# Kernel optimization log

Measured on AMD Instinct MI355X. Metric: run time of the kernel, lower is better.

The kernel has to match this reference:

```python
import jax, jax.numpy as jnp
import numpy as np

V, H, L, B, S = 32000, 1024, 2, 32, 512

def setup_inputs() -> dict:
    key = jax.random.key(0)
    ks = jax.random.split(key, 24)
    g = lambda k, shp, s=0.02: jax.random.normal(k, shp, dtype=jnp.float32) * s
    inp = {
        'input_ids': jax.random.randint(ks[0], (1, B), 0, V),
        'hidden': jax.random.normal(ks[1], (L, B, H), dtype=jnp.float32),
        'encoder_output': jax.random.normal(ks[2], (S, B, H), dtype=jnp.float32),
        'encoder_output_pinyin': jax.random.normal(ks[3], (S, B, H), dtype=jnp.float32),
        'embedding': g(ks[4], (V, H), 1.0),
        'W_ih0': g(ks[5], (3 * H, H)), 'W_hh0': g(ks[6], (3 * H, H)),
        'b_ih0': jnp.zeros((3 * H,), jnp.float32), 'b_hh0': jnp.zeros((3 * H,), jnp.float32),
        'W_ih1': g(ks[7], (3 * H, H)), 'W_hh1': g(ks[8], (3 * H, H)),
        'b_ih1': jnp.zeros((3 * H,), jnp.float32), 'b_hh1': jnp.zeros((3 * H,), jnp.float32),
        'att_fc1_w': g(ks[9], (H, 3 * H)), 'att_fc1_b': jnp.zeros((H,), jnp.float32),
        'att_fc2_w': g(ks[10], (1, H)), 'att_fc2_b': jnp.zeros((1,), jnp.float32),
        'attp_fc1_w': g(ks[11], (H, 3 * H)), 'attp_fc1_b': jnp.zeros((H,), jnp.float32),
        'attp_fc2_w': g(ks[12], (1, H)), 'attp_fc2_b': jnp.zeros((1,), jnp.float32),
        'attn_fc_w': g(ks[13], (H, 3 * H)), 'attn_fc_b': jnp.zeros((H,), jnp.float32),
        'fc_w': g(ks[14], (V, H)), 'fc_b': jnp.zeros((V,), jnp.float32),
    }
    return inp


def _gru_cell(x, h, Wih, Whh, bih, bhh):
    # torch GRU gate order: r, z, n
    gi = x @ Wih.T + bih          # [B, 3H]
    gh = h @ Whh.T + bhh          # [B, 3H]
    ir, iz, in_ = jnp.split(gi, 3, axis=-1)
    hr, hz, hn = jnp.split(gh, 3, axis=-1)
    r = jax.nn.sigmoid(ir + hr)
    z = jax.nn.sigmoid(iz + hz)
    n = jnp.tanh(in_ + r * hn)
    return (1.0 - z) * n + z * h


def _attention(hidden, enc, fc1_w, fc1_b, fc2_w, fc2_b):
    # hidden: [L, B, H], enc: [S, B, H]
    s, b = enc.shape[0], enc.shape[1]
    state = jnp.transpose(hidden, (1, 0, 2)).reshape(b, -1)       # [B, L*H]
    enc_b = jnp.transpose(enc, (1, 0, 2))                          # [B, S, H]
    state_rep = jnp.broadcast_to(state[:, None, :], (b, s, state.shape[-1]))
    concat = jnp.concatenate([state_rep, enc_b], axis=-1)          # [B, S, 3H]
    energy = jnp.tanh(concat @ fc1_w.T + fc1_b)                    # [B, S, H]
    energy = (energy @ fc2_w.T + fc2_b).transpose(0, 2, 1)         # [B, 1, S]
    alpha = jax.nn.softmax(energy, axis=2)
    context = jnp.einsum('bis,bsh->bih', alpha, enc_b)             # [B, 1, H]
    return jnp.transpose(context, (1, 0, 2)), alpha                # [1, B, H]


def reference(input_ids, hidden, encoder_output, encoder_output_pinyin, embedding,
              W_ih0, W_hh0, b_ih0, b_hh0, W_ih1, W_hh1, b_ih1, b_hh1,
              att_fc1_w, att_fc1_b, att_fc2_w, att_fc2_b,
              attp_fc1_w, attp_fc1_b, attp_fc2_w, attp_fc2_b,
              attn_fc_w, attn_fc_b, fc_w, fc_b):
    embedded = embedding[input_ids]             # [1, B, H] (dropout: eval mode = identity)
    x = embedded[0]                             # [B, H]
    h0 = _gru_cell(x, hidden[0], W_ih0, W_hh0, b_ih0, b_hh0)
    h1 = _gru_cell(h0, hidden[1], W_ih1, W_hh1, b_ih1, b_hh1)
    new_hidden = jnp.stack([h0, h1], axis=0)    # [L, B, H]
    output = h1[None]                           # [1, B, H]
    context, _ = _attention(new_hidden, encoder_output, att_fc1_w, att_fc1_b, att_fc2_w, att_fc2_b)
    context_p, _ = _attention(new_hidden, encoder_output_pinyin, attp_fc1_w, attp_fc1_b, attp_fc2_w, attp_fc2_b)
    fused = jnp.concatenate([output, context, context_p], axis=2)  # [1, B, 3H]
    output = jax.nn.relu(fused @ attn_fc_w.T + attn_fc_b)          # [1, B, H]
    logits = output @ fc_w.T + fc_b                                # [1, B, V]
    return logits, new_hidden
```

## Files before the change

### kernel.cpp

```cpp
#include <hip/hip_runtime.h>
#include <math.h>

#define Bsz 32
#define Hd  1024
#define Sd  512
#define Vd  32000

typedef __attribute__((ext_vector_type(8))) short v8s;
typedef __attribute__((ext_vector_type(4))) float v4f;

__device__ __forceinline__ float sigf(float x){ return 1.0f/(1.0f+__expf(-x)); }
__device__ __forceinline__ float ftanh(float x){
  float e = __expf(2.0f*x);
  return 1.0f - 2.0f/(e+1.0f);
}
__device__ __forceinline__ unsigned pk(float lo, float hi){
  return __builtin_amdgcn_perm(__float_as_uint(hi), __float_as_uint(lo), 0x07060302u);
}

__global__ void k_cvt_fc1w(const float* __restrict__ aw, const float* __restrict__ pw,
                           ushort* __restrict__ ab, ushort* __restrict__ pb){
  int tt = blockIdx.x*256 + threadIdx.x;
  int idx = tt*8;
  int s = idx >> 20;
  int r = idx & 1048575;
  int j = r >> 10, k = r & 1023;
  const float* src = (s? pw : aw) + (size_t)j*3072 + 2048 + k;
  float4 f0 = *(const float4*)src, f1 = *(const float4*)(src+4);
  uint4 p = { pk(f0.x,f0.y), pk(f0.z,f0.w), pk(f1.x,f1.y), pk(f1.z,f1.w) };
  *(uint4*)((s? pb : ab) + r) = p;
}

__global__ void k_embed(const int* __restrict__ ids, const float* __restrict__ emb,
                        float* __restrict__ x){
  int t = blockIdx.x*256 + threadIdx.x;
  int b = t >> 10, k = t & (Hd-1);
  x[t] = emb[(size_t)ids[b]*Hd + k];
}

__global__ void k_gates9(const float* __restrict__ x, const float* __restrict__ hid,
                         const float* __restrict__ Wih0, const float* __restrict__ Whh0,
                         const float* __restrict__ Whh1, float* __restrict__ gA){
  int blk = blockIdx.x;
  int g  = blk >> 9;
  int kc = (blk >> 7) & 3;
  int tt = (blk & 127)*256 + threadIdx.x;
  int b = tt & 31, j = tt >> 5;
  const float* vec; const float* w;
  if (g < 3){ vec = x + b*Hd; w = Wih0 + ((size_t)(g*Hd + j))*Hd; }
  else if (g < 6){ vec = hid + b*Hd; w = Whh0 + ((size_t)((g-3)*Hd + j))*Hd; }
  else { vec = hid + Bsz*Hd + b*Hd; w = Whh1 + ((size_t)((g-6)*Hd + j))*Hd; }
  const float4* v4 = (const float4*)(vec + kc*256);
  const float4* w4 = (const float4*)(w + kc*256);
  float acc = 0.f;
  #pragma unroll 8
  for (int k=0;k<64;k++){ float4 a=v4[k], ww=w4[k];
    acc += a.x*ww.x+a.y*ww.y+a.z*ww.z+a.w*ww.w; }
  atomicAdd(&gA[(size_t)g*32768 + j*32 + b], acc);
}

__global__ void k_gates3(const float* __restrict__ h0, const float* __restrict__ Wih1,
                         float* __restrict__ gB){
  int blk = blockIdx.x;
  int g  = blk >> 9;
  int kc = (blk >> 7) & 3;
  int tt = (blk & 127)*256 + threadIdx.x;
  int b = tt & 31, j = tt >> 5;
  const float4* v4 = (const float4*)(h0 + b*Hd + kc*256);
  const float4* w4 = (const float4*)(Wih1 + ((size_t)(g*Hd + j))*Hd + kc*256);
  float acc = 0.f;
  #pragma unroll 8
  for (int k=0;k<64;k++){ float4 a=v4[k], ww=w4[k];
    acc += a.x*ww.x+a.y*ww.y+a.z*ww.z+a.w*ww.w; }
  atomicAdd(&gB[(size_t)g*32768 + j*32 + b], acc);
}

__global__ void k_gru_comb(const float* __restrict__ xg, const float* __restrict__ hg,
                           const float* __restrict__ h, const float* __restrict__ bih,
                           const float* __restrict__ bhh, float* __restrict__ hnew){
  int tt = blockIdx.x*256 + threadIdx.x;
  int b = tt & 31, j = tt >> 5;
  float ir = xg[tt], iz = xg[32768 + tt], in_ = xg[2*32768 + tt];
  float hr = hg[tt], hz = hg[32768 + tt], hn  = hg[2*32768 + tt];
  float r = sigf(ir + bih[j]      + hr + bhh[j]);
  float z = sigf(iz + bih[Hd+j]   + hz + bhh[Hd+j]);
  float n = ftanh(in_ + bih[2*Hd+j] + r*(hn + bhh[2*Hd+j]));
  hnew[(size_t)b*Hd + j] = (1.f-z)*n + z*h[(size_t)b*Hd + j];
}

__global__ void k_spsplit(const float* __restrict__ h0, const float* __restrict__ h1,
                          const float* __restrict__ afc1w, const float* __restrict__ pfc1w,
                          float* __restrict__ spa_, float* __restrict__ spp_){
  int blk = blockIdx.x;
  int s  = blk >> 9;
  int kc = (blk >> 7) & 3;
  int tt = (blk & 127)*256 + threadIdx.x;
  int b = tt & 31, j = tt >> 5;
  const float* w = (s? pfc1w : afc1w) + (size_t)j*3*Hd + kc*512;
  const float* vec = (kc < 2 ? h0 : h1) + b*Hd + (kc & 1)*512;
  const float4* v4 = (const float4*)vec;
  const float4* w4 = (const float4*)w;
  float acc = 0.f;
  #pragma unroll 8
  for (int k=0;k<128;k++){ float4 a=v4[k], ww=w4[k];
    acc += a.x*ww.x+a.y*ww.y+a.z*ww.z+a.w*ww.w; }
  atomicAdd((s? spp_ : spa_) + (size_t)b*Hd + j, acc);
}

__global__ __launch_bounds__(256, 2)
void k_att_mfma(const float* __restrict__ enc0, const float* __restrict__ enc1,
                const ushort* __restrict__ wb0, const ushort* __restrict__ wb1,
                const float* __restrict__ sp0, const float* __restrict__ sp1,
                const float* __restrict__ b10, const float* __restrict__ b11,
                const float* __restrict__ w20, const float* __restrict__ w21,
                float* __restrict__ e0, float* __restrict__ e1){
  const int z = blockIdx.z;
  const float*  enc = z? enc1 : enc0;
  const ushort* wb  = z? wb1  : wb0;
  const float*  sp  = z? sp1  : sp0;
  const float*  b1  = z? b11  : b10;
  const float*  fc2 = z? w21  : w20;
  float* e = z? e1 : e0;
  __shared__ __align__(16) ushort As[128*72];
  __shared__ __align__(16) ushort Bs[128*72];
  const int t = threadIdx.x;
  const int lane = t & 63;
  const int w = t >> 6;
  const int wm = w >> 1, wn = w & 1;
  const int q = lane >> 4, c15 = lane & 15;
  const int row0 = blockIdx.y * 128;
  const int col0 = blockIdx.x * 128;

  const int lrow = t >> 3, lkp = (t & 7)*8;
  const float* gA = enc + (size_t)(row0 + lrow)*Hd + lkp;
  const int brow = t >> 1, bkp = (t & 1)*32;
  const ushort* gB = wb + (size_t)(col0 + brow)*Hd + bkp;

  v4f acc[4][4];
  for (int mi=0;mi<4;mi++) for (int ni=0;ni<4;ni++) acc[mi][ni] = (v4f){0.f,0.f,0.f,0.f};

  for (int k0 = 0; k0 < Hd; k0 += 64){
    #pragma unroll
    for (int i = 0; i < 4; i++){
      const float* p = gA + (size_t)i*32*Hd + k0;
      float4 a0 = *(const float4*)p;
      float4 a1 = *(const float4*)(p+4);
      uint4 pa = { pk(a0.x,a0.y), pk(a0.z,a0.w), pk(a1.x,a1.y), pk(a1.z,a1.w) };
      *(uint4*)&As[(i*32 + lrow)*72 + lkp] = pa;
    }
    {
      const uint4* pb4 = (const uint4*)(gB + k0);
      uint4 b0_=pb4[0], b1_=pb4[1], b2_=pb4[2], b3_=pb4[3];
      uint4* d = (uint4*)&Bs[brow*72 + bkp];
      d[0]=b0_; d[1]=b1_; d[2]=b2_; d[3]=b3_;
    }
    __syncthreads();
    #pragma unroll
    for (int kk = 0; kk < 2; kk++){
      v8s af[4], bf[4];
      #pragma unroll
      for (int mi=0;mi<4;mi++)
        af[mi] = *(const v8s*)&As[(wm*64 + mi*16 + c15)*72 + kk*32 + q*8];
      #pragma unroll
      for (int ni=0;ni<4;ni++)
        bf[ni] = *(const v8s*)&Bs[(wn*64 + ni*16 + c15)*72 + kk*32 + q*8];
      #pragma unroll
      for (int mi=0;mi<4;mi++)
        #pragma unroll
        for (int ni=0;ni<4;ni++)
          acc[mi][ni] = __builtin_amdgcn_mfma_f32_16x16x32_bf16(af[mi], bf[ni], acc[mi][ni], 0, 0, 0);
    }
    __syncthreads();
  }

  #pragma unroll
  for (int mi=0;mi<4;mi++){
    float rs[4] = {0.f,0.f,0.f,0.f};
    #pragma unroll
    for (int ni=0;ni<4;ni++){
      int col = col0 + wn*64 + ni*16 + c15;
      float w2 = fc2[col];
      float bb1 = b1[col];
      int bb = (mi & 1) * 16;
      #pragma unroll
      for (int r=0;r<4;r++){
        int b = bb + q*4 + r;
        float xv = acc[mi][ni][r] + sp[(size_t)b*Hd + col] + bb1;
        rs[r] += w2 * ftanh(xv);
      }
    }
    #pragma unroll
    for (int r=0;r<4;r++){
      float v = rs[r];
      v += __shfl_xor(v, 1);
      v += __shfl_xor(v, 2);
      v += __shfl_xor(v, 4);
      v += __shfl_xor(v, 8);
      if (c15 == 0)
        atomicAdd(&e[row0 + wm*64 + mi*16 + q*4 + r], v);
    }
  }
}

__global__ void k_softmax(float* __restrict__ ea_, float* __restrict__ ep_){
  float* e = blockIdx.y ? ep_ : ea_;
  const int b = blockIdx.x, t = threadIdx.x;
  __shared__ float red[256];
  float v1 = e[t*Bsz + b], v2 = e[(t+256)*Bsz + b];
  red[t] = fmaxf(v1, v2);
  __syncthreads();
  for (int off=128; off; off>>=1){ if (t<off) red[t]=fmaxf(red[t],red[t+off]); __syncthreads(); }
  float m = red[0];
  __syncthreads();
  float e1 = __expf(v1-m), e2 = __expf(v2-m);
  red[t] = e1 + e2;
  __syncthreads();
  for (int off=128; off; off>>=1){ if (t<off) red[t]+=red[t+off]; __syncthreads(); }
  float inv = 1.0f/red[0];
  e[t*Bsz + b] = e1*inv;
  e[(t+256)*Bsz + b] = e2*inv;
}

__global__ void k_context(const float* __restrict__ ea_, const float* __restrict__ ep_,
                          const float* __restrict__ enc0, const float* __restrict__ enc1,
                          float* __restrict__ ctx0, float* __restrict__ ctx1){
  const int z = blockIdx.z;
  const float* alpha = z? ep_ : ea_;
  const float* enc   = z? enc1 : enc0;
  float* ctx         = z? ctx1 : ctx0;
  const int b = blockIdx.x, c = blockIdx.y, t = threadIdx.x;
  float4 acc = {0,0,0,0};
  for (int s = c*64; s < c*64 + 64; s++){
    float a = alpha[s*Bsz + b];
    float4 ev = *(const float4*)(enc + (size_t)(s*Bsz+b)*Hd + t*4);
    acc.x += a*ev.x; acc.y += a*ev.y; acc.z += a*ev.z; acc.w += a*ev.w;
  }
  float* p = ctx + (size_t)b*Hd + t*4;
  atomicAdd(p+0, acc.x); atomicAdd(p+1, acc.y);
  atomicAdd(p+2, acc.z); atomicAdd(p+3, acc.w);
}

__global__ void k_fcsplit(const float* __restrict__ h1, const float* __restrict__ ctx,
                          const float* __restrict__ ctxp, const float* __restrict__ W,
                          float* __restrict__ o1acc){
  int blk = blockIdx.x;
  int c = blk >> 7;
  int tt = (blk & 127)*256 + threadIdx.x;
  int b = tt & 31, j = tt >> 5;
  int seg = c >> 2, off = (c & 3)*256;
  const float* vec = (seg==0 ? h1 : (seg==1 ? ctx : ctxp)) + b*Hd + off;
  const float* w = W + (size_t)j*3*Hd + seg*Hd + off;
  const float4* v4 = (const float4*)vec;
  const float4* w4 = (const float4*)w;
  float acc = 0.f;
  #pragma unroll 8
  for (int k=0;k<64;k++){ float4 a=v4[k], ww=w4[k];
    acc += a.x*ww.x+a.y*ww.y+a.z*ww.z+a.w*ww.w; }
  atomicAdd(&o1acc[(size_t)j*32 + b], acc);
}

__global__ void k_o1comb(const float* __restrict__ o1acc, const float* __restrict__ bias,
                         ushort* __restrict__ o1b){
  int tt = blockIdx.x*256 + threadIdx.x;
  int b = tt & 31, j = tt >> 5;
  float acc = fmaxf(o1acc[tt] + bias[j], 0.f);
  o1b[(size_t)b*Hd + j] = (ushort)(__float_as_uint(acc) >> 16);
}

__global__ __launch_bounds__(512)
void k_logits(const ushort* __restrict__ o1b, const float* __restrict__ fcw,
              const float* __restrict__ fcb, float* __restrict__ lg){
  __shared__ __align__(16) ushort Bs[128*72];
  const int t = threadIdx.x;
  const int lane = t & 63, w = t >> 6;
  const int q = lane >> 4, c15 = lane & 15;
  const int v0 = blockIdx.x * 128;
  const int scol = t >> 2, skq = (t & 3) * 16;
  const float* gB = fcw + (size_t)(v0 + scol)*Hd + skq;
  v4f acc[2] = {(v4f){0,0,0,0},(v4f){0,0,0,0}};
  for (int k0=0;k0<Hd;k0+=64){
    float4 f0 = *(const float4*)(gB + k0);
    float4 f1 = *(const float4*)(gB + k0 + 4);
    float4 f2 = *(const float4*)(gB + k0 + 8);
    float4 f3 = *(const float4*)(gB + k0 + 12);
    uint4 p0 = { pk(f0.x,f0.y), pk(f0.z,f0.w), pk(f1.x,f1.y), pk(f1.z,f1.w) };
    uint4 p1 = { pk(f2.x,f2.y), pk(f2.z,f2.w), pk(f3.x,f3.y), pk(f3.z,f3.w) };
    *(uint4*)&Bs[scol*72 + skq] = p0;
    *(uint4*)&Bs[scol*72 + skq + 8] = p1;
    __syncthreads();
    #pragma unroll
    for (int kk=0;kk<2;kk++){
      v8s bfrag = *(const v8s*)&Bs[(w*16 + c15)*72 + kk*32 + q*8];
      #pragma unroll
      for (int mf=0; mf<2; mf++){
        v8s afrag = *(const v8s*)(o1b + (size_t)(mf*16 + c15)*Hd + k0 + kk*32 + q*8);
        acc[mf] = __builtin_amdgcn_mfma_f32_16x16x32_bf16(afrag, bfrag, acc[mf], 0, 0, 0);
      }
    }
    __syncthreads();
  }
  int col = v0 + w*16 + c15;
  float bias = fcb[col];
  #pragma unroll
  for (int mf=0;mf<2;mf++)
    #pragma unroll
    for (int r=0;r<4;r++){
      int b = mf*16 + q*4 + r;
      lg[(size_t)b*Vd + col] = acc[mf][r] + bias;
    }
}

extern "C" void kernel_launch(void* const* d_in, const int* in_sizes, int n_in,
                              void* d_out, int out_size, void* d_ws, size_t ws_size,
                              hipStream_t stream) {
  const int*   ids  = (const int*)  d_in[0];
  const float* hid  = (const float*)d_in[1];
  const float* enc  = (const float*)d_in[2];
  const float* encp = (const float*)d_in[3];
  const float* emb  = (const float*)d_in[4];
  const float* Wih0 = (const float*)d_in[5];
  const float* Whh0 = (const float*)d_in[6];
  const float* bih0 = (const float*)d_in[7];
  const float* bhh0 = (const float*)d_in[8];
  const float* Wih1 = (const float*)d_in[9];
  const float* Whh1 = (const float*)d_in[10];
  const float* bih1 = (const float*)d_in[11];
  const float* bhh1 = (const float*)d_in[12];
  const float* afc1w= (const float*)d_in[13];
  const float* afc1b= (const float*)d_in[14];
  const float* afc2w= (const float*)d_in[15];
  const float* pfc1w= (const float*)d_in[17];
  const float* pfc1b= (const float*)d_in[18];
  const float* pfc2w= (const float*)d_in[19];
  const float* nfcw = (const float*)d_in[21];
  const float* nfcb = (const float*)d_in[22];
  const float* fcw  = (const float*)d_in[23];
  const float* fcb  = (const float*)d_in[24];

  float* outp   = (float*)d_out;
  float* logits = outp;
  float* h0     = outp + (size_t)Bsz*Vd;
  float* h1     = h0 + Bsz*Hd;

  float* ws = (float*)d_ws;
  ushort* fc1wab = (ushort*)ws;
  ushort* fc1wpb = (ushort*)(ws + 524288);
  float* x    = ws + 1048576;
  float* spa  = ws + 1081344;
  float* spp  = ws + 1114112;
  float* ea   = ws + 1146880;
  float* ep   = ws + 1163264;
  float* ctx  = ws + 1179648;
  float* ctxp = ws + 1212416;
  float* gA   = ws + 1245184;
  float* gB   = ws + 1540096;
  float* o1a  = ws + 1638400;
  ushort* o1b = (ushort*)(ws + 1671168);

  hipMemsetAsync(spa, 0, (size_t)589824*sizeof(float), stream);

  k_cvt_fc1w<<<1024, 256, 0, stream>>>(afc1w, pfc1w, fc1wab, fc1wpb);
  k_embed   <<<Bsz*Hd/256, 256, 0, stream>>>(ids, emb, x);
  k_gates9  <<<4608, 256, 0, stream>>>(x, hid, Wih0, Whh0, Whh1, gA);
  k_gru_comb<<<128, 256, 0, stream>>>(gA, gA + 3*32768, hid, bih0, bhh0, h0);
  k_gates3  <<<1536, 256, 0, stream>>>(h0, Wih1, gB);
  k_gru_comb<<<128, 256, 0, stream>>>(gB, gA + 6*32768, hid + Bsz*Hd, bih1, bhh1, h1);
  k_spsplit <<<1024, 256, 0, stream>>>(h0, h1, afc1w, pfc1w, spa, spp);

  dim3 ga(Hd/128, Sd*Bsz/128, 2);
  k_att_mfma<<<ga, 256, 0, stream>>>(enc, encp, fc1wab, fc1wpb, spa, spp,
                                     afc1b, pfc1b, afc2w, pfc2w, ea, ep);

  k_softmax<<<dim3(Bsz,2), 256, 0, stream>>>(ea, ep);
  k_context<<<dim3(Bsz,8,2), 256, 0, stream>>>(ea, ep, enc, encp, ctx, ctxp);

  k_fcsplit<<<1536, 256, 0, stream>>>(h1, ctx, ctxp, nfcw, o1a);
  k_o1comb <<<128, 256, 0, stream>>>(o1a, nfcb, o1b);
  k_logits <<<Vd/128, 512, 0, stream>>>(o1b, fcw, fcb, logits);
}
```

Before: 909.3 us.

## Remap attention blocks per XCD and load logits weights directly into MFMA fragments

Result: no change. 911.5 us (+0.2%).

```diff
diff --git a/kernel.cpp b/kernel.cpp
--- a/kernel.cpp
+++ b/kernel.cpp
@@ -107,14 +107,21 @@
   atomicAdd((s? spp_ : spa_) + (size_t)b*Hd + j, acc);
 }
 
-__global__ __launch_bounds__(256, 2)
+__global__ __launch_bounds__(256, 4)
 void k_att_mfma(const float* __restrict__ enc0, const float* __restrict__ enc1,
                 const ushort* __restrict__ wb0, const ushort* __restrict__ wb1,
                 const float* __restrict__ sp0, const float* __restrict__ sp1,
                 const float* __restrict__ b10, const float* __restrict__ b11,
                 const float* __restrict__ w20, const float* __restrict__ w21,
                 float* __restrict__ e0, float* __restrict__ e1){
-  const int z = blockIdx.z;
+  const int flat = blockIdx.x + (blockIdx.y << 3) + (blockIdx.z << 10);
+  const int xcd  = flat & 7;
+  const int widx = flat >> 3;
+  const int z    = widx >> 7;
+  const int rem  = widx & 127;
+  const int rowt = (xcd << 4) + (rem >> 3);
+  const int colb = rem & 7;
+
   const float*  enc = z? enc1 : enc0;
   const ushort* wb  = z? wb1  : wb0;
   const float*  sp  = z? sp1  : sp0;
@@ -128,8 +135,8 @@
   const int w = t >> 6;
   const int wm = w >> 1, wn = w & 1;
   const int q = lane >> 4, c15 = lane & 15;
-  const int row0 = blockIdx.y * 128;
-  const int col0 = blockIdx.x * 128;
+  const int row0 = rowt * 128;
+  const int col0 = colb * 128;
 
   const int lrow = t >> 3, lkp = (t & 7)*8;
   const float* gA = enc + (size_t)(row0 + lrow)*Hd + lkp;
@@ -270,36 +277,26 @@
 __global__ __launch_bounds__(512)
 void k_logits(const ushort* __restrict__ o1b, const float* __restrict__ fcw,
               const float* __restrict__ fcb, float* __restrict__ lg){
-  __shared__ __align__(16) ushort Bs[128*72];
   const int t = threadIdx.x;
   const int lane = t & 63, w = t >> 6;
   const int q = lane >> 4, c15 = lane & 15;
   const int v0 = blockIdx.x * 128;
-  const int scol = t >> 2, skq = (t & 3) * 16;
-  const float* gB = fcw + (size_t)(v0 + scol)*Hd + skq;
+  const int col = v0 + w*16 + c15;
+  const float*  gB  = fcw + (size_t)col*Hd + q*8;
+  const ushort* gA0 = o1b + (size_t)c15*Hd + q*8;
+  const ushort* gA1 = o1b + (size_t)(16 + c15)*Hd + q*8;
   v4f acc[2] = {(v4f){0,0,0,0},(v4f){0,0,0,0}};
-  for (int k0=0;k0<Hd;k0+=64){
-    float4 f0 = *(const float4*)(gB + k0);
-    float4 f1 = *(const float4*)(gB + k0 + 4);
-    float4 f2 = *(const float4*)(gB + k0 + 8);
-    float4 f3 = *(const float4*)(gB + k0 + 12);
-    uint4 p0 = { pk(f0.x,f0.y), pk(f0.z,f0.w), pk(f1.x,f1.y), pk(f1.z,f1.w) };
-    uint4 p1 = { pk(f2.x,f2.y), pk(f2.z,f2.w), pk(f3.x,f3.y), pk(f3.z,f3.w) };
-    *(uint4*)&Bs[scol*72 + skq] = p0;
-    *(uint4*)&Bs[scol*72 + skq + 8] = p1;
-    __syncthreads();
-    #pragma unroll
-    for (int kk=0;kk<2;kk++){
-      v8s bfrag = *(const v8s*)&Bs[(w*16 + c15)*72 + kk*32 + q*8];
-      #pragma unroll
-      for (int mf=0; mf<2; mf++){
-        v8s afrag = *(const v8s*)(o1b + (size_t)(mf*16 + c15)*Hd + k0 + kk*32 + q*8);
-        acc[mf] = __builtin_amdgcn_mfma_f32_16x16x32_bf16(afrag, bfrag, acc[mf], 0, 0, 0);
-      }
-    }
-    __syncthreads();
+  #pragma unroll 4
+  for (int k=0;k<Hd;k+=32){
+    float4 f0 = *(const float4*)(gB + k);
+    float4 f1 = *(const float4*)(gB + k + 4);
+    uint4 p = { pk(f0.x,f0.y), pk(f0.z,f0.w), pk(f1.x,f1.y), pk(f1.z,f1.w) };
+    v8s bfrag = *(const v8s*)&p;
+    v8s a0 = *(const v8s*)(gA0 + k);
+    v8s a1 = *(const v8s*)(gA1 + k);
+    acc[0] = __builtin_amdgcn_mfma_f32_16x16x32_bf16(a0, bfrag, acc[0], 0, 0, 0);
+    acc[1] = __builtin_amdgcn_mfma_f32_16x16x32_bf16(a1, bfrag, acc[1], 0, 0, 0);
   }
-  int col = v0 + w*16 + c15;
   float bias = fcb[col];
   #pragma unroll
   for (int mf=0;mf<2;mf++)
```
